# Performance work log

Measured on AMD Instinct MI355X. Metric: run time of the kernel, lower is better.

Reference implementation:

```python
import jax, jax.numpy as jnp
import numpy as np
from math import factorial

# ---- static config (mirrors CACE_LR defaults) ----
MAX_L, MAX_NU = 3, 3
N_RBF, N_RADIAL = 6, 6
N_BASIS = 3                       # n_atom_basis
N_CH = N_BASIS * N_BASIS          # edge channels = 9
CUTOFF, P = 5.5, 6
NZ = 94                           # elements with Z < 95
N_NODES, N_EDGES, N_GRAPHS = 10000, 80000, 16
MP_NORM = 1.0 / np.sqrt(10.0)     # 1/sqrt(avg_num_neighbors)

# Cartesian angular monomials x^lx y^ly z^lz with lx+ly+lz = l <= MAX_L
LXLYLZ = [(lx, ly, l - lx - ly) for l in range(MAX_L + 1)
          for lx in range(l, -1, -1) for ly in range(l - lx, -1, -1)]
N_ANG = len(LXLYLZ)               # 20
MONO = np.array(LXLYLZ, np.int32)
L_OF = MONO.sum(1)                # l of each monomial
IDX000 = LXLYLZ.index((0, 0, 0))
MIDX = {m: i for i, m in enumerate(LXLYLZ)}

def _mult(m):
    return factorial(sum(m)) / (factorial(m[0]) * factorial(m[1]) * factorial(m[2]))

MULT = np.array([_mult(m) for m in LXLYLZ], np.float32)
# nu=2 invariants: per l>=1, sum_m mult(m) * A_m^2
NU2_W = [np.where(L_OF == l, MULT, 0.0).astype(np.float32) for l in range(1, MAX_L + 1)]
# nu=3 invariants: pairs (l1,l2), contract A_m1 * A_m2 * A_{m1+m2}
NU3 = []
for (l1, l2) in [(1, 1), (1, 2)]:
    i1s, i2s, i12s, cfs = [], [], [], []
    for m1 in [m for m in LXLYLZ if sum(m) == l1]:
        for m2 in [m for m in LXLYLZ if sum(m) == l2]:
            m12 = (m1[0] + m2[0], m1[1] + m2[1], m1[2] + m2[2])
            i1s.append(MIDX[m1]); i2s.append(MIDX[m2]); i12s.append(MIDX[m12])
            cfs.append(_mult(m12))
    NU3.append((np.array(i1s), np.array(i2s), np.array(i12s), np.array(cfs, np.float32)))
N_SYM = 1 + MAX_L + len(NU3)      # 6 symmetrized angular features
FLAT_DIM = N_RADIAL * N_SYM * N_CH * 2  # 648


def monomials(u):                 # u: [E,3] unit vectors -> [E, N_ANG]
    pows = jnp.stack([jnp.ones_like(u), u, u * u, u * u * u], axis=1)  # [E,4,3]
    return pows[:, MONO[:, 0], 0] * pows[:, MONO[:, 1], 1] * pows[:, MONO[:, 2], 2]


def symmetrize(A):                # A: [N,R,N_ANG,C] -> B: [N,R,N_SYM,C]
    outs = [A[:, :, IDX000, :]]
    A2 = A * A
    for w in NU2_W:
        outs.append(jnp.einsum('nrac,a->nrc', A2, jnp.asarray(w)))
    for i1, i2, i12, cf in NU3:
        outs.append(jnp.einsum('nrkc,k->nrc', A[:, :, i1] * A[:, :, i2] * A[:, :, i12],
                               jnp.asarray(cf)))
    return jnp.stack(outs, axis=2)


def radial_tf(A, W):              # shared-per-l radial linear, W: [MAX_L+1,R,S]
    return jnp.einsum('nrac,ars->nsac', A, W[L_OF])


def setup_inputs() -> dict:
    key = jax.random.key(0)
    ks = jax.random.split(key, 16)
    pos = jax.random.uniform(ks[0], (N_NODES, 3), jnp.float32) * 10.0  # 10 A box
    node_type = jax.random.randint(ks[1], (N_NODES,), 0, NZ)
    src = jax.random.randint(ks[2], (N_EDGES,), 0, N_NODES)
    dst = jax.random.randint(ks[3], (N_EDGES,), 0, N_NODES)
    shifts = jnp.zeros((N_EDGES, 3), jnp.float32)
    batch_ids = jnp.sort(jax.random.randint(ks[4], (N_NODES,), 0, N_GRAPHS))
    s = lambda k, sh, f: jax.random.normal(k, sh, jnp.float32) * f
    params = dict(
        Wemb=s(ks[5], (NZ, N_BASIS), 0.5),
        freqs=jnp.arange(1, N_RBF + 1, dtype=jnp.float32) * np.pi / CUTOFF,
        W_rt=s(ks[6], (MAX_L + 1, N_RBF, N_RADIAL), 1 / np.sqrt(N_RBF)),
        W_mem=s(ks[7], (MAX_L + 1, N_RADIAL, N_RADIAL), 1 / np.sqrt(N_RADIAL)),
        W_Ar=s(ks[8], (MAX_L + 1, N_RBF, N_RADIAL), 1 / np.sqrt(N_RBF)),
        W_chi=s(ks[9], (N_RADIAL * N_SYM * N_CH, N_CH), 1 / np.sqrt(N_RADIAL * N_SYM * N_CH)),
        W1=s(ks[10], (FLAT_DIM, 64), 1 / np.sqrt(FLAT_DIM)),
        b1=jnp.zeros((64,), jnp.float32),
        W2=s(ks[11], (64, 32), 1 / 8.0),
        b2=jnp.zeros((32,), jnp.float32),
        W3=s(ks[12], (32, 1), 1 / np.sqrt(32.0)),
        b3=jnp.zeros((1,), jnp.float32),
    )
    return dict(pos=pos, node_type=node_type, src=src, dst=dst,
                shifts=shifts, batch_ids=batch_ids, **params)


def reference(pos, node_type, src, dst, shifts, batch_ids, Wemb, freqs,
              W_rt, W_mem, W_Ar, W_chi, W1, b1, W2, b2, W3, b3):
    n = pos.shape[0]
    # edge geometry (get_edge_vectors_and_lengths, normalize=True)
    vec = pos[dst] - pos[src] + shifts
    r = jnp.linalg.norm(vec, axis=-1, keepdims=True) + 1e-9           # [E,1]
    unit = vec / r
    # Bessel RBF and polynomial cutoff (p=6)
    rbf = jnp.sqrt(2.0 / CUTOFF) * jnp.sin(r * freqs[None]) / r      # [E,R]
    u = r[:, 0] / CUTOFF
    fc = jnp.where(u < 1.0,
                   1.0 - (P + 1) * (P + 2) / 2.0 * u**P + P * (P + 2) * u**(P + 1)
                   - P * (P + 1) / 2.0 * u**(P + 2), 0.0)
    radial = rbf * fc[:, None]
    ang = monomials(unit)                                             # [E,N_ANG]
    # node one-hot + embedding folded into a table lookup; directed edge encoding
    emb = Wemb[node_type]                                             # [N,3]
    edge_code = (emb[src][:, :, None] * emb[dst][:, None, :]).reshape(-1, N_CH)
    # edge_attri[e,r,a,c] = radial * angular * edge_code
    edge_attri = radial[:, :, None, None] * ang[:, None, :, None] * edge_code[:, None, None, :]
    A = radial_tf(jax.ops.segment_sum(edge_attri, dst, num_segments=n), W_rt)
    B = symmetrize(A)
    B_list = [B]
    # ---- one message-passing step: M (memory) + Ar + Bchi ----
    memory = radial_tf(A, W_mem)
    chi = B.reshape(n, -1) @ W_chi                                    # [N,C]
    msg_B = edge_attri * chi[src][:, None, None, :]
    A_B = radial_tf(jax.ops.segment_sum(msg_B, dst, num_segments=n), W_rt)
    rad_Ar = jnp.einsum('er,ars->eas', rbf, W_Ar[L_OF]) * fc[:, None, None]  # [E,A,S]
    msg_Ar = A[src] * jnp.transpose(rad_Ar, (0, 2, 1))[:, :, :, None]
    A_r = jax.ops.segment_sum(msg_Ar, dst, num_segments=n)
    A = (A_r + A_B) * MP_NORM + memory
    B_list.append(symmetrize(A))
    feats = jnp.stack(B_list, axis=-1).reshape(n, -1)                 # [N, 648]
    # MLP readout (atomwise_hidden=[64,32], num_targets=1), SiLU activations
    h = jax.nn.silu(feats @ W1 + b1)
    h = jax.nn.silu(h @ W2 + b2)
    atomic = h @ W3 + b3                                              # [N,1]
    return jnp.squeeze(jax.ops.segment_sum(atomic, batch_ids, num_segments=N_GRAPHS))
```

## Files before the change

### kernel.cpp

```cpp
#include <hip/hip_runtime.h>
#include <hip/hip_bf16.h>
#include <math.h>

#define NE 80000
#define NN 10000
#define NG 16
#define NBLK 157
#define MP_NORM 0.31622776601683794f
#define RBF_NORM 0.60302268915552724f

__constant__ int c_mx[20] = {0, 1,0,0, 2,1,1,0,0,0, 3,2,2,1,1,1,0,0,0,0};
__constant__ int c_my[20] = {0, 0,1,0, 0,1,0,2,1,0, 0,1,0,2,1,0,3,2,1,0};
__constant__ int c_mz[20] = {0, 0,0,1, 0,0,1,0,1,2, 0,0,1,0,1,2,0,1,2,3};

__device__ __forceinline__ int l_of_a(int a) {
    return (a >= 10) ? 3 : ((a >= 4) ? 2 : ((a >= 1) ? 1 : 0));
}

__device__ __forceinline__ void symm_from_lds2(const float2* Als2, float* brow,
                                               int lane) {
    if (lane >= 54) return;
    const int s2 = lane / 9, c = lane - s2 * 9;
    const float2* a = Als2 + (s2 >> 1) * 180 + c;
    const int hi = s2 & 1;
    float v[20];
    #pragma unroll
    for (int i = 0; i < 20; i++) {
        const float2 t = a[i * 9];
        v[i] = hi ? t.y : t.x;
    }
    const float o0 = v[0];
    const float o1 = v[1]*v[1] + v[2]*v[2] + v[3]*v[3];
    const float o2 = v[4]*v[4] + 2.f*v[5]*v[5] + 2.f*v[6]*v[6]
                   + v[7]*v[7] + 2.f*v[8]*v[8] + v[9]*v[9];
    const float o3 = v[10]*v[10] + 3.f*v[11]*v[11] + 3.f*v[12]*v[12]
                   + 3.f*v[13]*v[13] + 6.f*v[14]*v[14] + 3.f*v[15]*v[15]
                   + v[16]*v[16] + 3.f*v[17]*v[17] + 3.f*v[18]*v[18] + v[19]*v[19];
    const float o4 = v[1]*v[1]*v[4] + 2.f*v[1]*v[2]*v[5] + 2.f*v[1]*v[3]*v[6]
                   + 2.f*v[2]*v[1]*v[5] + v[2]*v[2]*v[7] + 2.f*v[2]*v[3]*v[8]
                   + 2.f*v[3]*v[1]*v[6] + 2.f*v[3]*v[2]*v[8] + v[3]*v[3]*v[9];
    const float o5 =
        v[1]*(v[4]*v[10] + 3.f*v[5]*v[11] + 3.f*v[6]*v[12] + 3.f*v[7]*v[13]
              + 6.f*v[8]*v[14] + 3.f*v[9]*v[15])
      + v[2]*(3.f*v[4]*v[11] + 3.f*v[5]*v[13] + 6.f*v[6]*v[14] + v[7]*v[16]
              + 3.f*v[8]*v[17] + 3.f*v[9]*v[18])
      + v[3]*(3.f*v[4]*v[12] + 6.f*v[5]*v[14] + 3.f*v[6]*v[15] + 3.f*v[7]*v[17]
              + 3.f*v[8]*v[18] + v[9]*v[19]);
    float* b = brow + s2 * 54 + c;
    b[0]  = o0;
    b[9]  = o1;
    b[18] = o2;
    b[27] = o3;
    b[36] = o4;
    b[45] = o5;
}

__global__ __launch_bounds__(256) void k_pack(
    const float* __restrict__ W1, const float* __restrict__ W_chi,
    float4* __restrict__ W1p, float2* __restrict__ WchiT2)
{
    const int idx = blockIdx.x * 256 + threadIdx.x;
    if (idx < 2 * 81 * 64) {
        const int h = idx / (81 * 64);
        const int r = idx - h * 81 * 64;
        const int g = r >> 6, lane = r & 63;
        float4 v;
        v.x = W1[(size_t)(8*g + 0 + h)*64 + lane];
        v.y = W1[(size_t)(8*g + 2 + h)*64 + lane];
        v.z = W1[(size_t)(8*g + 4 + h)*64 + lane];
        v.w = W1[(size_t)(8*g + 6 + h)*64 + lane];
        W1p[idx] = v;
    } else if (idx < 2*81*64 + 9*162) {
        const int r = idx - 2*81*64;
        const int cc = r / 162, j2 = r - cc * 162;
        WchiT2[(size_t)cc*162 + j2] = make_float2(W_chi[(2*j2)*9 + cc],
                                                  W_chi[(2*j2 + 1)*9 + cc]);
    }
}

__global__ __launch_bounds__(256) void k_hist(
    const float* __restrict__ pos, const int* __restrict__ src,
    const int* __restrict__ dst, const float* __restrict__ shifts,
    int* __restrict__ indeg)
{
    const int e = blockIdx.x * 256 + threadIdx.x;
    if (e >= NE) return;
    const int sn = src[e], dn = dst[e];
    const float vx = pos[3*dn+0] - pos[3*sn+0] + shifts[3*e+0];
    const float vy = pos[3*dn+1] - pos[3*sn+1] + shifts[3*e+1];
    const float vz = pos[3*dn+2] - pos[3*sn+2] + shifts[3*e+2];
    const float r = sqrtf(vx*vx + vy*vy + vz*vz) + 1e-9f;
    if (r * (1.0f / 5.5f) < 1.0f) atomicAdd(&indeg[dn], 1);
}

__global__ __launch_bounds__(256) void k_scan(const int* __restrict__ indeg,
                                              int* __restrict__ offs)
{
    __shared__ int part[256];
    const int t = threadIdx.x;
    int s = 0;
    for (int i = t * 40; i < t * 40 + 40; i++)
        if (i < NN) s += indeg[i];
    part[t] = s;
    __syncthreads();
    if (t == 0) {
        int run = 0;
        for (int i = 0; i < 256; i++) { int v = part[i]; part[i] = run; run += v; }
    }
    __syncthreads();
    int run = part[t];
    for (int i = t * 40; i < t * 40 + 40; i++) {
        if (i < NN) { offs[i] = run; run += indeg[i]; }
    }
}

__global__ __launch_bounds__(256) void k_fill(
    const float* __restrict__ pos, const int* __restrict__ src,
    const int* __restrict__ dst, const float* __restrict__ shifts,
    const int* __restrict__ ntype, const float* __restrict__ Wemb,
    const int* __restrict__ offs, int* __restrict__ cursor,
    int* __restrict__ esrc, float4* __restrict__ egeo,
    float* __restrict__ ecode)
{
    const int e = blockIdx.x * 256 + threadIdx.x;
    if (e >= NE) return;
    const int sn = src[e], dn = dst[e];
    const float vx = pos[3*dn+0] - pos[3*sn+0] + shifts[3*e+0];
    const float vy = pos[3*dn+1] - pos[3*sn+1] + shifts[3*e+1];
    const float vz = pos[3*dn+2] - pos[3*sn+2] + shifts[3*e+2];
    const float r = sqrtf(vx*vx + vy*vy + vz*vz) + 1e-9f;
    if (r * (1.0f / 5.5f) < 1.0f) {
        const int p = offs[dn] + atomicAdd(&cursor[dn], 1);
        esrc[p] = sn;
        const float inv = 1.0f / r;
        egeo[p] = make_float4(vx*inv, vy*inv, vz*inv, r);
        const int ts = ntype[sn], td = ntype[dn];
        const float es0 = Wemb[3*ts], es1 = Wemb[3*ts+1], es2 = Wemb[3*ts+2];
        const float ed0 = Wemb[3*td], ed1 = Wemb[3*td+1], ed2 = Wemb[3*td+2];
        float* cp = ecode + (size_t)p * 9;
        cp[0] = es0*ed0; cp[1] = es0*ed1; cp[2] = es0*ed2;
        cp[3] = es1*ed0; cp[4] = es1*ed1; cp[5] = es1*ed2;
        cp[6] = es2*ed0; cp[7] = es2*ed1; cp[8] = es2*ed2;
    }
}

__device__ __forceinline__ float gemv_packed(const float4* wp,
                                             const float* Bv, int lane) {
    float4 w0 = wp[(size_t)0*64 + lane];
    float4 w1 = wp[(size_t)1*64 + lane];
    float4 w2 = wp[(size_t)2*64 + lane];
    float s0 = 0.f, s1 = 0.f, s2 = 0.f, s3 = 0.f;
    for (int g = 0; g < 81; g += 3) {
        s0 = fmaf(Bv[4*g+ 0], w0.x, s0); s1 = fmaf(Bv[4*g+ 1], w0.y, s1);
        s2 = fmaf(Bv[4*g+ 2], w0.z, s2); s3 = fmaf(Bv[4*g+ 3], w0.w, s3);
        if (g + 3 < 81) w0 = wp[(size_t)(g+3)*64 + lane];
        s0 = fmaf(Bv[4*g+ 4], w1.x, s0); s1 = fmaf(Bv[4*g+ 5], w1.y, s1);
        s2 = fmaf(Bv[4*g+ 6], w1.z, s2); s3 = fmaf(Bv[4*g+ 7], w1.w, s3);
        if (g + 4 < 81) w1 = wp[(size_t)(g+4)*64 + lane];
        s0 = fmaf(Bv[4*g+ 8], w2.x, s0); s1 = fmaf(Bv[4*g+ 9], w2.y, s1);
        s2 = fmaf(Bv[4*g+10], w2.z, s2); s3 = fmaf(Bv[4*g+11], w2.w, s3);
        if (g + 5 < 81) w2 = wp[(size_t)(g+5)*64 + lane];
    }
    return (s0 + s1) + (s2 + s3);
}

__global__ __launch_bounds__(128) void k_node1(
    const float* __restrict__ freqs, const float* __restrict__ W_rt,
    const int* __restrict__ offs, const int* __restrict__ indeg,
    const int* __restrict__ esrc, const float4* __restrict__ egeo,
    const float* __restrict__ ecode, const float4* __restrict__ W1p,
    const float2* __restrict__ WchiT2,
    float2* __restrict__ A2, float* __restrict__ chi, float* __restrict__ P1)
{
    __shared__ float2 Als2S[2][540];
    __shared__ float  BlsS[2][324];
    const int tid = threadIdx.x;
    const int lane = tid & 63, w = tid >> 6;
    const int n = blockIdx.x * 2 + w;
    float2* Als2 = Als2S[w];
    float*  Bls  = BlsS[w];
    int aslot[3], cslot[3], rslot[3];
    float acc[3][6];
    #pragma unroll
    for (int j = 0; j < 3; j++) {
        const int p = lane + 64 * j;
        const int pc = (p < 180) ? p : 0;
        aslot[j] = pc / 9;
        cslot[j] = 20 + pc % 9;
        rslot[j] = 29 + 6 * l_of_a(pc / 9);
        #pragma unroll
        for (int s = 0; s < 6; s++) acc[j][s] = 0.f;
    }
    float fr[6];
    #pragma unroll
    for (int q = 0; q < 6; q++) fr[q] = freqs[q];
    float wrt[6];
    if (lane >= 29 && lane < 53) {
        const int j = lane - 29, l = j / 6, s2 = j % 6;
        #pragma unroll
        for (int q = 0; q < 6; q++) wrt[q] = W_rt[(l*6 + q)*6 + s2];
    }
    int mlx = 0, mly = 0, mlz = 0;
    if (lane < 20) { mlx = c_mx[lane]; mly = c_my[lane]; mlz = c_mz[lane]; }
    const int e0 = offs[n], cnt = indeg[n];
    float4 geo = make_float4(0.f, 0.f, 0.f, 1.f);
    float ecd = 0.f;
    if (cnt > 0) {
        geo = egeo[e0];
        if (lane >= 20 && lane < 29) ecd = ecode[(size_t)e0*9 + lane - 20];
    }
    for (int t = 0; t < cnt; t++) {
        const float4 g = geo;
        const float ec = ecd;
        if (t + 1 < cnt) {
            geo = egeo[e0 + t + 1];
            if (lane >= 20 && lane < 29)
                ecd = ecode[(size_t)(e0 + t + 1)*9 + lane - 20];
        }
        float regX = ec;
        if (lane < 20) {
            float v = 1.f;
            for (int i = 0; i < mlx; i++) v *= g.x;
            for (int i = 0; i < mly; i++) v *= g.y;
            for (int i = 0; i < mlz; i++) v *= g.z;
            regX = v;
        } else if (lane >= 29 && lane < 53) {
            const float r = g.w;
            const float u = r * (1.0f / 5.5f);
            const float u2 = u*u, u3 = u2*u, u6 = u3*u3;
            const float fcv = 1.0f - 28.0f*u6 + 48.0f*u6*u - 21.0f*u6*u2;
            const float inv = fcv / r;
            float s = 0.f;
            #pragma unroll
            for (int q = 0; q < 6; q++)
                s += RBF_NORM * __sinf(r * fr[q]) * inv * wrt[q];
            regX = s;
        }
        float pp[3];
        #pragma unroll
        for (int j = 0; j < 3; j++)
            pp[j] = __shfl(regX, aslot[j]) * __shfl(regX, cslot[j]);
        #pragma unroll
        for (int j = 0; j < 3; j++) {
            #pragma unroll
            for (int s = 0; s < 6; s++)
                acc[j][s] = fmaf(__shfl(regX, rslot[j] + s), pp[j], acc[j][s]);
        }
    }
    #pragma unroll
    for (int j = 0; j < 3; j++) {
        const int p = lane + 64 * j;
        if (p < 180) {
            #pragma unroll
            for (int sp = 0; sp < 3; sp++) {
                const float2 v = make_float2(acc[j][2*sp], acc[j][2*sp+1]);
                A2[(size_t)n*540 + sp*180 + p] = v;
                Als2[sp*180 + p] = v;
            }
        }
    }
    symm_from_lds2(Als2, Bls, lane);
    {
        float s = 0.f;
        if (lane < 54) {
            const int cc = lane % 9, gg = lane / 9;
            const float2* wc = WchiT2 + (size_t)cc * 162 + gg * 27;
            const int jb = gg * 54;
            float2 c0 = wc[0];
            float2 c1 = wc[1];
            for (int i = 0; i < 27; i += 2) {
                s = fmaf(Bls[jb + 2*i    ], c0.x, s);
                s = fmaf(Bls[jb + 2*i + 1], c0.y, s);
                if (i + 2 < 27) c0 = wc[i + 2];
                if (i + 1 < 27) {
                    s = fmaf(Bls[jb + 2*i + 2], c1.x, s);
                    s = fmaf(Bls[jb + 2*i + 3], c1.y, s);
                    if (i + 3 < 27) c1 = wc[i + 3];
                }
            }
        }
        const float t1 = __shfl(s, lane + 27);
        if (lane < 27) s += t1;
        const float t2 = __shfl(s, lane + 9);
        const float t3 = __shfl(s, lane + 18);
        if (lane < 9) chi[(size_t)n * 9 + lane] = s + t2 + t3;
    }
    P1[(size_t)n*64 + lane] = gemv_packed(W1p, Bls, lane);
}

__global__ __launch_bounds__(128) void k_node2(
    const float* __restrict__ freqs, const float* __restrict__ W_rt,
    const float* __restrict__ W_Ar, const float* __restrict__ W_mem,
    const int* __restrict__ offs, const int* __restrict__ indeg,
    const int* __restrict__ esrc, const float4* __restrict__ egeo,
    const float* __restrict__ ecode, const float* __restrict__ chi,
    const float2* __restrict__ A2, const float4* __restrict__ W1p,
    float* __restrict__ P2)
{
    __shared__ float2 Als2S[2][540];
    __shared__ float  B2lsS[2][324];
    __shared__ float  WmS[2][144];
    const int tid = threadIdx.x;
    const int lane = tid & 63, w = tid >> 6;
    const int n = blockIdx.x * 2 + w;
    float2* Als2 = Als2S[w];
    float*  B2ls = B2lsS[w];
    float*  Wm   = WmS[w];
    #pragma unroll
    for (int k = 0; k < 9; k++) {
        const int i = lane + 64 * k;
        if (i < 540) Als2[i] = A2[(size_t)n*540 + i];
    }
    Wm[lane] = W_mem[lane];
    Wm[lane + 64] = W_mem[lane + 64];
    if (lane < 16) Wm[lane + 128] = W_mem[lane + 128];
    int aslot[3], cslot[3], rslot[3];
    float acc[3][6];
    #pragma unroll
    for (int j = 0; j < 3; j++) {
        const int p = lane + 64 * j;
        const int pc = (p < 180) ? p : 0;
        aslot[j] = pc / 9;
        cslot[j] = 20 + pc % 9;
        rslot[j] = 29 + 6 * l_of_a(pc / 9);
        #pragma unroll
        for (int s = 0; s < 6; s++) acc[j][s] = 0.f;
    }
    float fr[6];
    #pragma unroll
    for (int q = 0; q < 6; q++) fr[q] = freqs[q];
    float wrtB[6], wrtA[6];
    if (lane >= 29 && lane < 53) {
        const int j = lane - 29, l = j / 6, s2 = j % 6;
        #pragma unroll
        for (int q = 0; q < 6; q++) {
            wrtB[q] = W_rt[(l*6 + q)*6 + s2];
            wrtA[q] = W_Ar[(l*6 + q)*6 + s2];
        }
    }
    int mlx = 0, mly = 0, mlz = 0;
    if (lane < 20) { mlx = c_mx[lane]; mly = c_my[lane]; mlz = c_mz[lane]; }
    const int e0 = offs[n], cnt = indeg[n];
    int sn2 = 0;
    float4 geo = make_float4(0.f, 0.f, 0.f, 1.f);
    float ecd = 0.f, chin = 0.f;
    float an[3][6];
    #pragma unroll
    for (int j = 0; j < 3; j++)
        #pragma unroll
        for (int s = 0; s < 6; s++) an[j][s] = 0.f;
    if (cnt > 0) {
        const int sn1 = esrc[e0];
        geo = egeo[e0];
        if (lane >= 20 && lane < 29) {
            ecd  = ecode[(size_t)e0*9 + lane - 20];
            chin = chi[(size_t)sn1*9 + lane - 20];
        }
        const float2* ar = A2 + (size_t)sn1 * 540;
        #pragma unroll
        for (int j = 0; j < 3; j++) {
            const int p = lane + 64 * j;
            if (p < 180) {
                #pragma unroll
                for (int sp = 0; sp < 3; sp++) {
                    const float2 t2 = ar[sp*180 + p];
                    an[j][2*sp] = t2.x; an[j][2*sp+1] = t2.y;
                }
            }
        }
    }
    if (cnt > 1) sn2 = esrc[e0 + 1];
    for (int t = 0; t < cnt; t++) {
        const float4 g = geo;
        const float ec = ecd, ch = chin;
        float av[3][6];
        #pragma unroll
        for (int j = 0; j < 3; j++)
            #pragma unroll
            for (int s = 0; s < 6; s++) av[j][s] = an[j][s];
        if (t + 1 < cnt) {
            geo = egeo[e0 + t + 1];
            if (lane >= 20 && lane < 29) {
                ecd  = ecode[(size_t)(e0 + t + 1)*9 + lane - 20];
                chin = chi[(size_t)sn2*9 + lane - 20];
            }
            const float2* ar = A2 + (size_t)sn2 * 540;
            #pragma unroll
            for (int j = 0; j < 3; j++) {
                const int p = lane + 64 * j;
                if (p < 180) {
                    #pragma unroll
                    for (int sp = 0; sp < 3; sp++) {
                        const float2 t2 = ar[sp*180 + p];
                        an[j][2*sp] = t2.x; an[j][2*sp+1] = t2.y;
                    }
                }
            }
            if (t + 2 < cnt) sn2 = esrc[e0 + t + 2];
        }
        float regX = ec * ch;
        float regY = 0.f;
        if (lane < 20) {
            float v = 1.f;
            for (int i = 0; i < mlx; i++) v *= g.x;
            for (int i = 0; i < mly; i++) v *= g.y;
            for (int i = 0; i < mlz; i++) v *= g.z;
            regX = v;
        } else if (lane >= 29 && lane < 53) {
            const float r = g.w;
            const float u = r * (1.0f / 5.5f);
            const float u2 = u*u, u3 = u2*u, u6 = u3*u3;
            const float fcv = 1.0f - 28.0f*u6 + 48.0f*u6*u - 21.0f*u6*u2;
            const float inv = fcv / r;
            float sB = 0.f, sA = 0.f;
            #pragma unroll
            for (int q = 0; q < 6; q++) {
                const float rb = RBF_NORM * __sinf(r * fr[q]) * inv;
                sB = fmaf(rb, wrtB[q], sB);
                sA = fmaf(rb, wrtA[q], sA);
            }
            regX = sB;
            regY = sA;
        }
        float pp[3];
        #pragma unroll
        for (int j = 0; j < 3; j++)
            pp[j] = __shfl(regX, aslot[j]) * __shfl(regX, cslot[j]);
        #pragma unroll
        for (int j = 0; j < 3; j++) {
            #pragma unroll
            for (int s = 0; s < 6; s++) {
                const float rB = __shfl(regX, rslot[j] + s);
                const float rA = __shfl(regY, rslot[j] + s);
                acc[j][s] += rB * pp[j] + av[j][s] * rA;
            }
        }
    }
    #pragma unroll
    for (int j = 0; j < 3; j++) {
        const int p = lane + 64 * j;
        if (p < 180) {
            const int l = l_of_a(p / 9);
            float a6[6];
            #pragma unroll
            for (int sp = 0; sp < 3; sp++) {
                const float2 t2 = Als2[sp*180 + p];
                a6[2*sp] = t2.x; a6[2*sp+1] = t2.y;
            }
            float mv[6];
            #pragma unroll
            for (int s = 0; s < 6; s++) {
                float m = 0.f;
                #pragma unroll
                for (int sp = 0; sp < 6; sp++)
                    m = fmaf(a6[sp], Wm[l*36 + sp*6 + s], m);
                mv[s] = acc[j][s] * MP_NORM + m;
            }
            #pragma unroll
            for (int sp = 0; sp < 3; sp++)
                Als2[sp*180 + p] = make_float2(mv[2*sp], mv[2*sp+1]);
        }
    }
    symm_from_lds2(Als2, B2ls, lane);
    P2[(size_t)n*64 + lane] = gemv_packed(W1p + (size_t)81*64, B2ls, lane);
}

__global__ __launch_bounds__(256) void k_tail(
    const float* __restrict__ P1, const float* __restrict__ P2,
    const float* __restrict__ b1, const float* __restrict__ W2,
    const float* __restrict__ b2, const float* __restrict__ W3,
    const float* __restrict__ b3, const int* __restrict__ batch,
    float* __restrict__ part)
{
    __shared__ float h1s[64][66];
    __shared__ float W2L[2048];
    __shared__ float gsum[16];
    const int tid = threadIdx.x;
    const int nb = blockIdx.x * 64;
    if (tid < 16) gsum[tid] = 0.f;
    for (int idx = tid; idx < 2048; idx += 256) W2L[idx] = W2[idx];
    for (int idx = tid; idx < 4096; idx += 256) {
        const int nl = idx >> 6, o = idx & 63;
        float h = 0.f;
        if (nb + nl < NN)
            h = P1[(size_t)(nb + nl)*64 + o] + P2[(size_t)(nb + nl)*64 + o]
              + b1[o];
        h1s[nl][o] = h / (1.f + __expf(-h));
    }
    __syncthreads();
    const int nl = tid >> 2, og = (tid & 3) * 8;
    float acc2[8];
    #pragma unroll
    for (int j = 0; j < 8; j++) acc2[j] = b2[og + j];
    #pragma unroll 8
    for (int k = 0; k < 64; k++) {
        const float hv = h1s[nl][k];
        const float4 wA = *(const float4*)&W2L[k*32 + og];
        const float4 wB = *(const float4*)&W2L[k*32 + og + 4];
        acc2[0] = fmaf(hv, wA.x, acc2[0]); acc2[1] = fmaf(hv, wA.y, acc2[1]);
        acc2[2] = fmaf(hv, wA.z, acc2[2]); acc2[3] = fmaf(hv, wA.w, acc2[3]);
        acc2[4] = fmaf(hv, wB.x, acc2[4]); acc2[5] = fmaf(hv, wB.y, acc2[5]);
        acc2[6] = fmaf(hv, wB.z, acc2[6]); acc2[7] = fmaf(hv, wB.w, acc2[7]);
    }
    float s = 0.f;
    #pragma unroll
    for (int j = 0; j < 8; j++) {
        const float g = acc2[j] / (1.f + __expf(-acc2[j]));
        s = fmaf(g, W3[og + j], s);
    }
    s += __shfl_xor(s, 1);
    s += __shfl_xor(s, 2);
    if ((tid & 3) == 0 && nb + nl < NN)
        atomicAdd(&gsum[batch[nb + nl]], s + b3[0]);
    __syncthreads();
    if (tid < 16) part[blockIdx.x * 16 + tid] = gsum[tid];
}

__global__ __launch_bounds__(64) void k_final(const float* __restrict__ part,
                                              float* __restrict__ out)
{
    const int t = threadIdx.x;
    if (t >= 16) return;
    float acc = 0.f;
    for (int b = 0; b < NBLK; b++) acc += part[b * 16 + t];
    out[t] = acc;
}

extern "C" void kernel_launch(void* const* d_in, const int* in_sizes, int n_in,
                              void* d_out, int out_size, void* d_ws, size_t ws_size,
                              hipStream_t stream)
{
    const float* pos    = (const float*)d_in[0];
    const int*   ntype  = (const int*)  d_in[1];
    const int*   src    = (const int*)  d_in[2];
    const int*   dst    = (const int*)  d_in[3];
    const float* shifts = (const float*)d_in[4];
    const int*   batch  = (const int*)  d_in[5];
    const float* Wemb   = (const float*)d_in[6];
    const float* freqs  = (const float*)d_in[7];
    const float* W_rt   = (const float*)d_in[8];
    const float* W_mem  = (const float*)d_in[9];
    const float* W_Ar   = (const float*)d_in[10];
    const float* W_chi  = (const float*)d_in[11];
    const float* W1     = (const float*)d_in[12];
    const float* b1     = (const float*)d_in[13];
    const float* W2     = (const float*)d_in[14];
    const float* b2     = (const float*)d_in[15];
    const float* W3     = (const float*)d_in[16];
    const float* b3     = (const float*)d_in[17];

    float*  ws    = (float*)d_ws;
    float2* A2    = (float2*)ws;
    float*  P1    = ws   + (size_t)NN * 1080;
    float*  P2    = P1   + (size_t)NN * 64;
    float*  chi   = P2   + (size_t)NN * 64;
    float4* egeo  = (float4*)(chi + (size_t)NN * 9);
    int*    esrc  = (int*)(egeo + NE);
    float*  ecode = (float*)(esrc + NE);
    float*  part  = ecode + (size_t)NE * 9;
    int*    indeg  = (int*)(part + NBLK * 16);
    int*    offs   = indeg  + 10240;
    int*    cursor = offs   + 10240;
    float4* W1p    = (float4*)(cursor + 10240);
    float2* WchiT2 = (float2*)(W1p + 2*81*64);

    hipMemsetAsync(indeg,  0, 10240 * sizeof(int), stream);
    hipMemsetAsync(cursor, 0, 10240 * sizeof(int), stream);

    k_pack<<<48, 256, 0, stream>>>(W1, W_chi, W1p, WchiT2);
    k_hist<<<(NE + 255)/256, 256, 0, stream>>>(pos, src, dst, shifts, indeg);
    k_scan<<<1, 256, 0, stream>>>(indeg, offs);
    k_fill<<<(NE + 255)/256, 256, 0, stream>>>(pos, src, dst, shifts, ntype,
                                               Wemb, offs, cursor, esrc, egeo,
                                               ecode);
    k_node1<<<NN/2, 128, 0, stream>>>(freqs, W_rt, offs, indeg, esrc, egeo,
                                      ecode, W1p, WchiT2, A2, chi, P1);
    k_node2<<<NN/2, 128, 0, stream>>>(freqs, W_rt, W_Ar, W_mem, offs, indeg,
                                      esrc, egeo, ecode, chi, A2, W1p, P2);
    k_tail<<<NBLK, 256, 0, stream>>>(P1, P2, b1, W2, b2, W3, b3, batch, part);
    k_final<<<1, 64, 0, stream>>>(part, (float*)d_out);
}
```

Measured before the change: 175.3 us.

## Merge weight packing into histogram kernel, fold final reduce into tail, deepen GEMV prefetch

Weight packing now runs as extra blocks of the histogram kernel, and the final per-graph reduction is done by the last tail block through an atomic ticket. The two memsets are merged into one. Together these drop two kernel launches and one memset. The node GEMV and chi dot-product loops now prefetch six (or four) weight vectors ahead, with zero-padded LDS tails so the loops can overrun, which hides more load latency at the cost of extra registers.

```diff
diff --git a/kernel.cpp b/kernel.cpp
--- a/kernel.cpp
+++ b/kernel.cpp
@@ -55,42 +55,42 @@
     b[45] = o5;
 }
 
-__global__ __launch_bounds__(256) void k_pack(
-    const float* __restrict__ W1, const float* __restrict__ W_chi,
-    float4* __restrict__ W1p, float2* __restrict__ WchiT2)
-{
-    const int idx = blockIdx.x * 256 + threadIdx.x;
-    if (idx < 2 * 81 * 64) {
-        const int h = idx / (81 * 64);
-        const int r = idx - h * 81 * 64;
-        const int g = r >> 6, lane = r & 63;
-        float4 v;
-        v.x = W1[(size_t)(8*g + 0 + h)*64 + lane];
-        v.y = W1[(size_t)(8*g + 2 + h)*64 + lane];
-        v.z = W1[(size_t)(8*g + 4 + h)*64 + lane];
-        v.w = W1[(size_t)(8*g + 6 + h)*64 + lane];
-        W1p[idx] = v;
-    } else if (idx < 2*81*64 + 9*162) {
-        const int r = idx - 2*81*64;
-        const int cc = r / 162, j2 = r - cc * 162;
-        WchiT2[(size_t)cc*162 + j2] = make_float2(W_chi[(2*j2)*9 + cc],
-                                                  W_chi[(2*j2 + 1)*9 + cc]);
-    }
-}
-
 __global__ __launch_bounds__(256) void k_hist(
     const float* __restrict__ pos, const int* __restrict__ src,
     const int* __restrict__ dst, const float* __restrict__ shifts,
-    int* __restrict__ indeg)
-{
-    const int e = blockIdx.x * 256 + threadIdx.x;
-    if (e >= NE) return;
-    const int sn = src[e], dn = dst[e];
-    const float vx = pos[3*dn+0] - pos[3*sn+0] + shifts[3*e+0];
-    const float vy = pos[3*dn+1] - pos[3*sn+1] + shifts[3*e+1];
-    const float vz = pos[3*dn+2] - pos[3*sn+2] + shifts[3*e+2];
-    const float r = sqrtf(vx*vx + vy*vy + vz*vz) + 1e-9f;
-    if (r * (1.0f / 5.5f) < 1.0f) atomicAdd(&indeg[dn], 1);
+    int* __restrict__ indeg, const float* __restrict__ W1,
+    const float* __restrict__ W_chi, float4* __restrict__ W1p,
+    float2* __restrict__ WchiT2)
+{
+    const int b = blockIdx.x;
+    if (b < 313) {
+        const int e = b * 256 + threadIdx.x;
+        if (e >= NE) return;
+        const int sn = src[e], dn = dst[e];
+        const float vx = pos[3*dn+0] - pos[3*sn+0] + shifts[3*e+0];
+        const float vy = pos[3*dn+1] - pos[3*sn+1] + shifts[3*e+1];
+        const float vz = pos[3*dn+2] - pos[3*sn+2] + shifts[3*e+2];
+        const float r = sqrtf(vx*vx + vy*vy + vz*vz) + 1e-9f;
+        if (r * (1.0f / 5.5f) < 1.0f) atomicAdd(&indeg[dn], 1);
+    } else {
+        const int idx = (b - 313) * 256 + threadIdx.x;
+        if (idx < 2 * 81 * 64) {
+            const int h = idx / (81 * 64);
+            const int r = idx - h * 81 * 64;
+            const int g = r >> 6, lane = r & 63;
+            float4 v;
+            v.x = W1[(size_t)(8*g + 0 + h)*64 + lane];
+            v.y = W1[(size_t)(8*g + 2 + h)*64 + lane];
+            v.z = W1[(size_t)(8*g + 4 + h)*64 + lane];
+            v.w = W1[(size_t)(8*g + 6 + h)*64 + lane];
+            W1p[idx] = v;
+        } else if (idx < 2*81*64 + 9*162) {
+            const int r = idx - 2*81*64;
+            const int cc = r / 162, j2 = r - cc * 162;
+            WchiT2[(size_t)cc*162 + j2] = make_float2(W_chi[(2*j2)*9 + cc],
+                                                      W_chi[(2*j2 + 1)*9 + cc]);
+        }
+    }
 }
 
 __global__ __launch_bounds__(256) void k_scan(const int* __restrict__ indeg,
@@ -144,22 +144,22 @@
     }
 }
 
-__device__ __forceinline__ float gemv_packed(const float4* wp,
-                                             const float* Bv, int lane) {
-    float4 w0 = wp[(size_t)0*64 + lane];
-    float4 w1 = wp[(size_t)1*64 + lane];
-    float4 w2 = wp[(size_t)2*64 + lane];
+__device__ __forceinline__ float gemv_packed6(const float4* wp,
+                                              const float* Bv, int lane) {
+    float4 w[6];
+    #pragma unroll
+    for (int u = 0; u < 6; u++) w[u] = wp[(size_t)u*64 + lane];
     float s0 = 0.f, s1 = 0.f, s2 = 0.f, s3 = 0.f;
-    for (int g = 0; g < 81; g += 3) {
-        s0 = fmaf(Bv[4*g+ 0], w0.x, s0); s1 = fmaf(Bv[4*g+ 1], w0.y, s1);
-        s2 = fmaf(Bv[4*g+ 2], w0.z, s2); s3 = fmaf(Bv[4*g+ 3], w0.w, s3);
-        if (g + 3 < 81) w0 = wp[(size_t)(g+3)*64 + lane];
-        s0 = fmaf(Bv[4*g+ 4], w1.x, s0); s1 = fmaf(Bv[4*g+ 5], w1.y, s1);
-        s2 = fmaf(Bv[4*g+ 6], w1.z, s2); s3 = fmaf(Bv[4*g+ 7], w1.w, s3);
-        if (g + 4 < 81) w1 = wp[(size_t)(g+4)*64 + lane];
-        s0 = fmaf(Bv[4*g+ 8], w2.x, s0); s1 = fmaf(Bv[4*g+ 9], w2.y, s1);
-        s2 = fmaf(Bv[4*g+10], w2.z, s2); s3 = fmaf(Bv[4*g+11], w2.w, s3);
-        if (g + 5 < 81) w2 = wp[(size_t)(g+5)*64 + lane];
+    for (int g = 0; g < 84; g += 6) {
+        #pragma unroll
+        for (int u = 0; u < 6; u++) {
+            const int gg = g + u;
+            s0 = fmaf(Bv[4*gg+0], w[u].x, s0);
+            s1 = fmaf(Bv[4*gg+1], w[u].y, s1);
+            s2 = fmaf(Bv[4*gg+2], w[u].z, s2);
+            s3 = fmaf(Bv[4*gg+3], w[u].w, s3);
+            if (g + 6 + u < 81) w[u] = wp[(size_t)(g + 6 + u)*64 + lane];
+        }
     }
     return (s0 + s1) + (s2 + s3);
 }
@@ -173,12 +173,13 @@
     float2* __restrict__ A2, float* __restrict__ chi, float* __restrict__ P1)
 {
     __shared__ float2 Als2S[2][540];
-    __shared__ float  BlsS[2][324];
+    __shared__ float  BlsS[2][336];
     const int tid = threadIdx.x;
     const int lane = tid & 63, w = tid >> 6;
     const int n = blockIdx.x * 2 + w;
     float2* Als2 = Als2S[w];
     float*  Bls  = BlsS[w];
+    if (lane < 12) Bls[324 + lane] = 0.f;
     int aslot[3], cslot[3], rslot[3];
     float acc[3][6];
     #pragma unroll
@@ -266,16 +267,16 @@
             const int cc = lane % 9, gg = lane / 9;
             const float2* wc = WchiT2 + (size_t)cc * 162 + gg * 27;
             const int jb = gg * 54;
-            float2 c0 = wc[0];
-            float2 c1 = wc[1];
-            for (int i = 0; i < 27; i += 2) {
-                s = fmaf(Bls[jb + 2*i    ], c0.x, s);
-                s = fmaf(Bls[jb + 2*i + 1], c0.y, s);
-                if (i + 2 < 27) c0 = wc[i + 2];
-                if (i + 1 < 27) {
-                    s = fmaf(Bls[jb + 2*i + 2], c1.x, s);
-                    s = fmaf(Bls[jb + 2*i + 3], c1.y, s);
-                    if (i + 3 < 27) c1 = wc[i + 3];
+            float2 c[4];
+            #pragma unroll
+            for (int u = 0; u < 4; u++) c[u] = wc[u];
+            for (int i = 0; i < 28; i += 4) {
+                #pragma unroll
+                for (int u = 0; u < 4; u++) {
+                    const int ii = i + u;
+                    s = fmaf(Bls[jb + 2*ii    ], c[u].x, s);
+                    s = fmaf(Bls[jb + 2*ii + 1], c[u].y, s);
+                    if (i + 4 + u < 27) c[u] = wc[i + 4 + u];
                 }
             }
         }
@@ -285,7 +286,7 @@
         const float t3 = __shfl(s, lane + 18);
         if (lane < 9) chi[(size_t)n * 9 + lane] = s + t2 + t3;
     }
-    P1[(size_t)n*64 + lane] = gemv_packed(W1p, Bls, lane);
+    P1[(size_t)n*64 + lane] = gemv_packed6(W1p, Bls, lane);
 }
 
 __global__ __launch_bounds__(128) void k_node2(
@@ -298,7 +299,7 @@
     float* __restrict__ P2)
 {
     __shared__ float2 Als2S[2][540];
-    __shared__ float  B2lsS[2][324];
+    __shared__ float  B2lsS[2][336];
     __shared__ float  WmS[2][144];
     const int tid = threadIdx.x;
     const int lane = tid & 63, w = tid >> 6;
@@ -306,6 +307,7 @@
     float2* Als2 = Als2S[w];
     float*  B2ls = B2lsS[w];
     float*  Wm   = WmS[w];
+    if (lane < 12) B2ls[324 + lane] = 0.f;
     #pragma unroll
     for (int k = 0; k < 9; k++) {
         const int i = lane + 64 * k;
@@ -462,7 +464,7 @@
         }
     }
     symm_from_lds2(Als2, B2ls, lane);
-    P2[(size_t)n*64 + lane] = gemv_packed(W1p + (size_t)81*64, B2ls, lane);
+    P2[(size_t)n*64 + lane] = gemv_packed6(W1p + (size_t)81*64, B2ls, lane);
 }
 
 __global__ __launch_bounds__(256) void k_tail(
@@ -470,11 +472,13 @@
     const float* __restrict__ b1, const float* __restrict__ W2,
     const float* __restrict__ b2, const float* __restrict__ W3,
     const float* __restrict__ b3, const int* __restrict__ batch,
-    float* __restrict__ part)
+    float* __restrict__ part, int* __restrict__ ticket,
+    float* __restrict__ out)
 {
     __shared__ float h1s[64][66];
     __shared__ float W2L[2048];
     __shared__ float gsum[16];
+    __shared__ int isLast;
     const int tid = threadIdx.x;
     const int nb = blockIdx.x * 64;
     if (tid < 16) gsum[tid] = 0.f;
@@ -514,16 +518,18 @@
         atomicAdd(&gsum[batch[nb + nl]], s + b3[0]);
     __syncthreads();
     if (tid < 16) part[blockIdx.x * 16 + tid] = gsum[tid];
-}
-
-__global__ __launch_bounds__(64) void k_final(const float* __restrict__ part,
-                                              float* __restrict__ out)
-{
-    const int t = threadIdx.x;
-    if (t >= 16) return;
-    float acc = 0.f;
-    for (int b = 0; b < NBLK; b++) acc += part[b * 16 + t];
-    out[t] = acc;
+    __threadfence();
+    if (tid == 0) {
+        const int t = atomicAdd(ticket, 1);
+        isLast = (t == NBLK - 1) ? 1 : 0;
+    }
+    __syncthreads();
+    if (isLast && tid < 16) {
+        const volatile float* vp = part;
+        float acc = 0.f;
+        for (int b = 0; b < NBLK; b++) acc += vp[b * 16 + tid];
+        out[tid] = acc;
+    }
 }
 
 extern "C" void kernel_launch(void* const* d_in, const int* in_sizes, int n_in,
@@ -559,16 +565,16 @@
     float*  ecode = (float*)(esrc + NE);
     float*  part  = ecode + (size_t)NE * 9;
     int*    indeg  = (int*)(part + NBLK * 16);
-    int*    offs   = indeg  + 10240;
-    int*    cursor = offs   + 10240;
-    float4* W1p    = (float4*)(cursor + 10240);
+    int*    cursor = indeg  + 10240;
+    int*    ticket = cursor + 10240;
+    int*    offs   = ticket + 256;
+    float4* W1p    = (float4*)(offs + 10240);
     float2* WchiT2 = (float2*)(W1p + 2*81*64);
 
-    hipMemsetAsync(indeg,  0, 10240 * sizeof(int), stream);
-    hipMemsetAsync(cursor, 0, 10240 * sizeof(int), stream);
-
-    k_pack<<<48, 256, 0, stream>>>(W1, W_chi, W1p, WchiT2);
-    k_hist<<<(NE + 255)/256, 256, 0, stream>>>(pos, src, dst, shifts, indeg);
+    hipMemsetAsync(indeg, 0, (10240 + 10240 + 256) * sizeof(int), stream);
+
+    k_hist<<<361, 256, 0, stream>>>(pos, src, dst, shifts, indeg, W1, W_chi,
+                                    W1p, WchiT2);
     k_scan<<<1, 256, 0, stream>>>(indeg, offs);
     k_fill<<<(NE + 255)/256, 256, 0, stream>>>(pos, src, dst, shifts, ntype,
                                                Wemb, offs, cursor, esrc, egeo,
@@ -577,6 +583,6 @@
                                       ecode, W1p, WchiT2, A2, chi, P1);
     k_node2<<<NN/2, 128, 0, stream>>>(freqs, W_rt, W_Ar, W_mem, offs, indeg,
                                       esrc, egeo, ecode, chi, A2, W1p, P2);
-    k_tail<<<NBLK, 256, 0, stream>>>(P1, P2, b1, W2, b2, W3, b3, batch, part);
-    k_final<<<1, 64, 0, stream>>>(part, (float*)d_out);
-}
+    k_tail<<<NBLK, 256, 0, stream>>>(P1, P2, b1, W2, b2, W3, b3, batch, part,
+                                     ticket, (float*)d_out);
+}
```

Result: slower. 195.0 us (+11.2%).
